# Performance work log

Measured on AMD Instinct MI355X. Metric: run time of the kernel, lower is better.

## Reference

```python
import jax, jax.numpy as jnp
import numpy as np

H = 1024; NH = 16; L = 4; K = 128; N = 65536
ADIM_MOVE = 9; ADIM_TURN = 4; S = 2 * K + 2


def setup_inputs() -> dict:
    key = jax.random.key(0)
    ks = jax.random.split(key, 24)
    s = 0.02
    d = {}
    d['x'] = jax.random.normal(ks[0], (1, H), jnp.float32)
    d['memory_vectors'] = jax.random.normal(ks[1], (N, H), jnp.float32)
    d['memory_next_vectors'] = jax.random.normal(ks[2], (N, H), jnp.float32)
    d['memory_surprises'] = jax.random.uniform(ks[3], (N,), jnp.float32)
    d['memory_rewards'] = jax.random.normal(ks[4], (N,), jnp.float32)
    d['rand_noise'] = jax.random.uniform(ks[5], (N,), jnp.float32)
    d['action_idx_move'] = jax.random.randint(ks[6], (N,), 0, ADIM_MOVE)
    d['action_idx_turn'] = jax.random.randint(ks[7], (N,), 0, ADIM_TURN)
    d['start_token'] = jax.random.uniform(ks[8], (1, H)) * 2 - 1
    d['pos_emb'] = jax.random.uniform(ks[9], (S, H)) * 2 - 1
    d['in_proj_w'] = jax.random.normal(ks[10], (L, 3 * H, H)) * s
    d['in_proj_b'] = jnp.zeros((L, 3 * H))
    d['out_w'] = jax.random.normal(ks[11], (L, H, H)) * s
    d['out_b'] = jnp.zeros((L, H))
    d['ln1_w'] = jnp.ones((L, H)); d['ln1_b'] = jnp.zeros((L, H))
    d['ln2_w'] = jnp.ones((L, H)); d['ln2_b'] = jnp.zeros((L, H))
    d['ffn_w1'] = jax.random.normal(ks[12], (L, 4 * H, H)) * s
    d['ffn_b1'] = jnp.zeros((L, 4 * H))
    d['ffn_w2'] = jax.random.normal(ks[13], (L, H, 4 * H)) * s
    d['ffn_b2'] = jnp.zeros((L, H))
    d['act_move_w1'] = jax.random.normal(ks[14], (H, ADIM_MOVE)) * s
    d['act_move_b1'] = jnp.zeros((H,))
    d['act_move_w2'] = jax.random.normal(ks[15], (H, H)) * s
    d['act_move_b2'] = jnp.zeros((H,))
    d['act_turn_w1'] = jax.random.normal(ks[16], (H, ADIM_TURN)) * s
    d['act_turn_b1'] = jnp.zeros((H,))
    d['act_turn_w2'] = jax.random.normal(ks[17], (H, H)) * s
    d['act_turn_b2'] = jnp.zeros((H,))
    d['vh_w1'] = jax.random.normal(ks[18], (4 * H, H)) * s
    d['vh_b1'] = jnp.zeros((4 * H,))
    d['vh_w2'] = jax.random.normal(ks[19], (1, 4 * H)) * s
    d['vh_b2'] = jnp.zeros((1,))
    return d


def _get_scores(v):
    # tie-aware average rank / N (matches torch unique_consecutive logic)
    srt = jnp.sort(v)
    left = jnp.searchsorted(srt, v, side='left')
    right = jnp.searchsorted(srt, v, side='right')
    return ((left + right - 1).astype(v.dtype) / 2) / v.shape[0]


def _ln(x, w, b):
    m = x.mean(-1, keepdims=True)
    var = ((x - m) ** 2).mean(-1, keepdims=True)
    return (x - m) / jnp.sqrt(var + 1e-5) * w + b


def _gelu(x):
    return jax.nn.gelu(x, approximate=False)


def _mha(x, wqkv, bqkv, wo, bo, mask):
    dh = H // NH
    qkv = x @ wqkv.T + bqkv                      # [S, 3H]
    q, k, v = jnp.split(qkv, 3, axis=-1)
    q = q.reshape(-1, NH, dh); k = k.reshape(-1, NH, dh); v = v.reshape(-1, NH, dh)
    att = jnp.einsum('qhd,khd->hqk', q, k) / np.sqrt(dh).astype(np.float32)
    att = jax.nn.softmax(att + mask, axis=-1)
    o = jnp.einsum('hqk,khd->qhd', att, v).reshape(-1, H)
    return o @ wo.T + bo


def reference(x, memory_vectors, memory_next_vectors, memory_surprises, memory_rewards, rand_noise, action_idx_move, action_idx_turn, start_token, pos_emb, in_proj_w, in_proj_b, out_w, out_b, ln1_w, ln1_b, ln2_w, ln2_b, ffn_w1, ffn_b1, ffn_w2, ffn_b2, act_move_w1, act_move_b1, act_move_w2, act_move_b2, act_turn_w1, act_turn_b1, act_turn_w2, act_turn_b2, vh_w1, vh_b1, vh_w2, vh_b2):
    eps = 1e-8
    # ---- scoring (no_grad in original) ----
    xs = jax.lax.stop_gradient(x)
    xn = xs / jnp.maximum(jnp.linalg.norm(xs, axis=-1, keepdims=True), eps)
    mn = memory_vectors / jnp.maximum(jnp.linalg.norm(memory_vectors, axis=-1, keepdims=True), eps)
    sim = mn @ xn[0]                              # [N]
    scores = _get_scores(memory_surprises) ** 2 + _get_scores(sim) ** 2 + _get_scores(rand_noise) ** 2
    _, idx = jax.lax.top_k(scores, K)             # [K]
    # ---- gather memories + action one-hots ----
    sel = jax.lax.stop_gradient(memory_vectors[idx])   # [K, H]
    oh_move = jax.nn.one_hot(action_idx_move[idx], ADIM_MOVE, dtype=x.dtype)
    oh_turn = jax.nn.one_hot(action_idx_turn[idx], ADIM_TURN, dtype=x.dtype)
    av_move = _gelu(oh_move @ act_move_w1.T + act_move_b1) @ act_move_w2.T + act_move_b2
    av_turn = _gelu(oh_turn @ act_turn_w1.T + act_turn_b1) @ act_turn_w2.T + act_turn_b2
    av = (av_move + av_turn) / 2                  # mean over actions
    # interleave [v0, a0, v1, a1, ...], prepend start, append target
    vecs = jnp.stack((sel, av), axis=1).reshape(-1, H)
    vecs = jnp.concatenate((start_token, vecs, x), axis=0)   # [S, H]
    vecs = vecs + pos_emb
    mask = jnp.where(jnp.tril(jnp.ones((S, S), bool)), 0.0, -jnp.inf).astype(x.dtype)
    for l in range(L):
        vecs = vecs + _mha(_ln(vecs, ln1_w[l], ln1_b[l]), in_proj_w[l], in_proj_b[l], out_w[l], out_b[l], mask)
        h = _ln(vecs, ln2_w[l], ln2_b[l])
        vecs = vecs + _gelu(h @ ffn_w1[l].T + ffn_b1[l]) @ ffn_w2[l].T + ffn_b2[l]
    vidx = jnp.arange(K + 1) * 2 + 1
    vh_in = vecs[vidx]
    vp = _gelu(vh_in @ vh_w1.T + vh_b1) @ vh_w2.T + vh_b2   # [K+1, 1]
    sel_rewards = memory_rewards[idx]
    losses = (vp[:-1].ravel() - sel_rewards) ** 2            # mse, reduction='none'
    return (vecs[1:], memory_next_vectors[idx], vp[-1], losses, sel_rewards)
```

## Files before the change

### kernel.cpp

```cpp
#include <hip/hip_runtime.h>
#include <hip/hip_bf16.h>
#include <math.h>
#include <stdint.h>

typedef unsigned int u32;
typedef unsigned short u16;
typedef unsigned long long u64;

#define NM   65536
#define HD   1024
#define KS   128
#define SQ   258
#define NL   4
#define NBIN 65536
#define CCAP 2048

using bf16x8 = __attribute__((ext_vector_type(8))) short;
using f32x4v = __attribute__((ext_vector_type(4))) float;

static constexpr size_t A256(size_t x){ return (x + 255) & ~(size_t)255; }

constexpr size_t OFF_H3   = 0;
constexpr size_t OFF_C3   = OFF_H3 + (size_t)3*NBIN*4;
constexpr size_t OFF_HS   = OFF_C3 + (size_t)3*NBIN*4;
constexpr size_t ZERO_BYTES = OFF_HS + (size_t)NBIN*4;
constexpr u32 ZBLK = 1792;
constexpr size_t OFF_BS   = A256(ZERO_BYTES);
constexpr size_t OFF_P3   = A256(OFF_BS + 192*4);
constexpr size_t OFF_K3   = A256(OFF_P3 + (size_t)3*(NBIN+1)*4);
constexpr size_t OFF_L3   = A256(OFF_K3 + (size_t)3*NM*4);
constexpr size_t OFF_KSC  = A256(OFF_L3 + (size_t)3*NM*4);
constexpr size_t OFF_IDX  = A256(OFF_KSC + (size_t)NM*4);
constexpr size_t OFF_REW  = A256(OFF_IDX  + (size_t)KS*4);
constexpr size_t OFF_HM   = A256(OFF_REW  + (size_t)KS*4);
constexpr size_t OFF_HT   = A256(OFF_HM   + (size_t)KS*HD*2);
constexpr size_t OFF_VECS = A256(OFF_HT   + (size_t)KS*HD*2);
constexpr size_t OFF_LNB  = A256(OFF_VECS + (size_t)SQ*HD*4);
constexpr size_t OFF_QKV  = A256(OFF_LNB  + (size_t)SQ*HD*2);
constexpr size_t OFF_ATT  = A256(OFF_QKV  + (size_t)SQ*3*HD*2);
constexpr size_t OFF_FFH  = A256(OFF_ATT  + (size_t)SQ*HD*2);
constexpr size_t OFF_VHIN = A256(OFF_FFH  + (size_t)SQ*4*HD*2);
constexpr size_t OFF_WB   = A256(OFF_VHIN + (size_t)129*HD*2);
constexpr size_t NWELEM   = 56623104;
constexpr size_t OFF_PART = A256(OFF_WB + NWELEM*2);

constexpr size_t WB_IN = 0;
constexpr size_t WB_O  = WB_IN + (size_t)4*3*HD*HD;
constexpr size_t WB_F1 = WB_O  + (size_t)4*HD*HD;
constexpr size_t WB_F2 = WB_F1 + (size_t)4*4*HD*HD;
constexpr size_t WB_AM = WB_F2 + (size_t)4*4*HD*HD;
constexpr size_t WB_AT = WB_AM + (size_t)HD*HD;
constexpr size_t WB_VH = WB_AT + (size_t)HD*HD;

constexpr int OUT_NEXT = 257*HD;
constexpr int OUT_VP   = OUT_NEXT + KS*HD;
constexpr int OUT_LOSS = OUT_VP + 1;
constexpr int OUT_REWO = OUT_LOSS + KS;

struct Ctrl { u32 b1, above1, T, candcnt; };

__device__ __forceinline__ float gelu_f(float v){
  return 0.5f*v*(1.0f + erff(v*0.70710678118654752440f));
}

__device__ __forceinline__ u16 f2bf(float f){
  __hip_bfloat16 h = __float2bfloat16(f);
  u16 s; __builtin_memcpy(&s, &h, sizeof(u16));
  return s;
}

__device__ __forceinline__ float bf2f(u16 v){ return __uint_as_float(((u32)v) << 16); }

__device__ __forceinline__ float4 unpk4(u64 pk){
  u32 lo = (u32)pk, hi = (u32)(pk >> 32);
  float4 v;
  v.x = __uint_as_float(lo << 16);
  v.y = __uint_as_float(lo & 0xFFFF0000u);
  v.z = __uint_as_float(hi << 16);
  v.w = __uint_as_float(hi & 0xFFFF0000u);
  return v;
}

__device__ __forceinline__ u64 pk4(float4 v){
  u16 r[4] = { f2bf(v.x), f2bf(v.y), f2bf(v.z), f2bf(v.w) };
  u64 pk; __builtin_memcpy(&pk, r, 8);
  return pk;
}

__device__ __forceinline__ u32 fkey(float v){
  u32 b = __float_as_uint(v);
  return (b >> 31) ? ~b : (b | 0x80000000u);
}

__device__ __forceinline__ void gload16(const u16* g, u16* l){
  __builtin_amdgcn_global_load_lds(
      (const __attribute__((address_space(1))) unsigned int*)g,
      (__attribute__((address_space(3))) unsigned int*)l, 16, 0, 0);
}

struct WSeg { const float* s; u16* d; u32 base4, end4; };
struct WCA { WSeg seg[7]; u32 tot4; u32* z; };
__global__ __launch_bounds__(256) void k_wconv(WCA a){
  if(blockIdx.x < ZBLK) a.z[blockIdx.x*256 + threadIdx.x] = 0u;
  u32 i = blockIdx.x*256 + threadIdx.x;
  if(i >= a.tot4) return;
  #pragma unroll
  for(int j=0;j<7;++j){
    if(i < a.seg[j].end4){
      u32 off = i - a.seg[j].base4;
      float4 v = *(const float4*)&a.seg[j].s[(size_t)off*4];
      *(u64*)&a.seg[j].d[(size_t)off*4] = pk4(v);
      return;
    }
  }
}

__global__ __launch_bounds__(256) void k_simkey(const float* __restrict__ mv, const float* __restrict__ x,
                                                const float* __restrict__ surp, const float* __restrict__ noise,
                                                u32* __restrict__ keys3, u32* __restrict__ hist3){
  __shared__ float xs[HD];
  __shared__ float red[256];
  int t = threadIdx.x;
  float s = 0.f;
  for(int i=t;i<HD;i+=256){ float v=x[i]; s += v*v; }
  red[t]=s; __syncthreads();
  for(int o=128;o>0;o>>=1){ if(t<o) red[t]+=red[t+o]; __syncthreads(); }
  float nrm = fmaxf(sqrtf(red[0]), 1e-8f);
  for(int i=t;i<HD;i+=256) xs[i] = x[i]/nrm;
  __syncthreads();
  int lane = t & 63, w = t >> 6;
  #pragma unroll
  for(int rep=0;rep<2;++rep){
    int row = blockIdx.x*8 + rep*4 + w;
    const float4* p = (const float4*)(mv + (size_t)row*HD);
    const float4* q = (const float4*)xs;
    float d=0.f, ss=0.f;
    #pragma unroll
    for(int r=0;r<4;++r){
      float4 v = p[lane + 64*r]; float4 u = q[lane + 64*r];
      d  += v.x*u.x + v.y*u.y + v.z*u.z + v.w*u.w;
      ss += v.x*v.x + v.y*v.y + v.z*v.z + v.w*v.w;
    }
    for(int off=32;off>0;off>>=1){ d += __shfl_xor(d,off,64); ss += __shfl_xor(ss,off,64); }
    if(lane==0){
      float sim = d / fmaxf(sqrtf(ss),1e-8f);
      float vals[3] = { surp[row], sim, noise[row] };
      #pragma unroll
      for(int a=0;a<3;++a){
        u32 k = fkey(vals[a]);
        keys3[(size_t)a*NM + row] = k;
        atomicAdd(&hist3[(size_t)a*NBIN + (k >> 16)], 1u);
      }
    }
  }
}

__global__ __launch_bounds__(256) void k_scanA(const u32* __restrict__ hist3, u32* __restrict__ bsum){
  __shared__ u32 red[256];
  int blk = blockIdx.x;
  int t = threadIdx.x;
  const u32* h = hist3 + (size_t)(blk>>6)*NBIN + (size_t)(blk&63)*1024;
  u32 s = 0;
  #pragma unroll
  for(int j=0;j<4;++j) s += h[t*4+j];
  red[t]=s; __syncthreads();
  for(int o=128;o>0;o>>=1){ if(t<o) red[t]+=red[t+o]; __syncthreads(); }
  if(t==0) bsum[blk] = red[0];
}

__global__ __launch_bounds__(256) void k_scanC(const u32* __restrict__ hist3, const u32* __restrict__ bsum,
                                               u32* __restrict__ pref3){
  __shared__ u32 part[256];
  int blk = blockIdx.x;
  int t = threadIdx.x;
  int a = blk >> 6, c = blk & 63;
  u32 base = 0;
  for(int j=0;j<c;++j) base += bsum[a*64 + j];
  const u32* h = hist3 + (size_t)a*NBIN + (size_t)c*1024;
  u32* pref = pref3 + (size_t)a*(NBIN+1) + (size_t)c*1024;
  u32 loc[4]; u32 s = 0;
  #pragma unroll
  for(int j=0;j<4;++j){ loc[j] = h[t*4+j]; s += loc[j]; }
  part[t] = s; __syncthreads();
  for(int off=1;off<256;off<<=1){
    u32 u = (t >= off) ? part[t-off] : 0u;
    __syncthreads(); part[t] += u; __syncthreads();
  }
  u32 run = base + part[t] - s;
  #pragma unroll
  for(int j=0;j<4;++j){ pref[t*4+j] = run; run += loc[j]; }
  if(c == 63 && t == 255) pref3[(size_t)a*(NBIN+1) + NBIN] = NM;
}

__global__ void k_scatter3(const u32* __restrict__ keys3, const u32* __restrict__ pref3,
                           u32* __restrict__ cnt3, u32* __restrict__ lo3){
  int i = blockIdx.x*256 + threadIdx.x;
  if(i >= NM) return;
  #pragma unroll
  for(int a=0;a<3;++a){
    u32 k = keys3[(size_t)a*NM + i];
    u32 b = k >> 16;
    u32 pos = pref3[(size_t)a*(NBIN+1) + b] + atomicAdd(&cnt3[(size_t)a*NBIN + b], 1u);
    lo3[(size_t)a*NM + pos] = k & 0xFFFFu;
  }
}

__global__ void k_rank3score(const u32* __restrict__ keys3, const u32* __restrict__ pref3,
                             const u32* __restrict__ lo3, u32* __restrict__ keysS, u32* __restrict__ histS){
  int i = blockIdx.x*256 + threadIdx.x;
  if(i >= NM) return;
  float rr[3];
  #pragma unroll
  for(int a=0;a<3;++a){
    u32 k = keys3[(size_t)a*NM + i];
    u32 b = k >> 16, my = k & 0xFFFFu;
    const u32* pref = pref3 + (size_t)a*(NBIN+1);
    const u32* lo = lo3 + (size_t)a*NM;
    u32 s = pref[b], e = pref[b+1];
    u32 nl = 0, ne = 0;
    for(u32 j=s;j<e;++j){ u32 u = lo[j]; nl += (u < my); ne += (u == my); }
    u32 left = s + nl, right = left + ne;
    rr[a] = (float)(left + right - 1) * (1.0f/131072.0f);
  }
  float sc = __fadd_rn(__fadd_rn(__fmul_rn(rr[0],rr[0]), __fmul_rn(rr[1],rr[1])), __fmul_rn(rr[2],rr[2]));
  u32 k = __float_as_uint(sc);
  keysS[i] = k;
  atomicAdd(&histS[k >> 16], 1u);
}

__global__ __launch_bounds__(1024) void k_selsort(const u32* __restrict__ histS, const u32* __restrict__ keysS,
                                                  int* __restrict__ idx){
  __shared__ u32 part[1024];
  __shared__ u64 sm[CCAP];
  __shared__ u32 thrT, cnt;
  int t = threadIdx.x;
  u32 base = t*64, s = 0;
  for(int j=0;j<64;++j) s += histS[base+j];
  part[t] = s; __syncthreads();
  for(int off=1;off<1024;off<<=1){
    u32 v = (t+off < 1024) ? part[t+off] : 0u;
    __syncthreads(); part[t] += v; __syncthreads();
  }
  u32 above = part[t] - s;
  if(above < (u32)KS && above + s >= (u32)KS){
    u32 cum = above;
    for(int j=63;j>=0;--j){
      u32 c = histS[base+j];
      if(cum + c >= (u32)KS){ thrT = (u32)(base+j) << 16; cnt = 0; break; }
      cum += c;
    }
  }
  __syncthreads();
  u32 T = thrT;
  for(int i=t;i<NM;i+=1024){
    u32 k = keysS[i];
    if(k >= T){
      u32 p = atomicAdd(&cnt, 1u);
      if(p < (u32)CCAP) sm[p] = ((u64)(~k) << 32) | (u32)i;
    }
  }
  __syncthreads();
  u32 n = cnt; if(n > (u32)CCAP) n = CCAP;
  for(int i=t;i<CCAP;i+=1024) if(i >= (int)n) sm[i] = 0xFFFFFFFFFFFFFFFFull;
  __syncthreads();
  for(int k=2;k<=CCAP;k<<=1){
    for(int j=k>>1;j>0;j>>=1){
      for(int i=t;i<CCAP;i+=1024){
        int ixj = i ^ j;
        if(ixj > i){
          bool up = ((i & k) == 0);
          u64 a = sm[i], b = sm[ixj];
          if((a > b) == up){ sm[i] = b; sm[ixj] = a; }
        }
      }
      __syncthreads();
    }
  }
  if(t < KS) idx[t] = (int)(sm[t] & 0xFFFFFFFFu);
}

__global__ void k_gather(const int* __restrict__ idx,
                         const float* __restrict__ mv, const float* __restrict__ mnv,
                         const float* __restrict__ mrew,
                         const int* __restrict__ aim, const int* __restrict__ ait,
                         const float* __restrict__ amw1, const float* __restrict__ amb1,
                         const float* __restrict__ atw1, const float* __restrict__ atb1,
                         const float* __restrict__ start, const float* __restrict__ x,
                         const float* __restrict__ pos,
                         float* __restrict__ vecs, float* __restrict__ outnext,
                         u16* __restrict__ hm, u16* __restrict__ ht,
                         float* __restrict__ rew, float* __restrict__ outrew){
  int k = blockIdx.x;
  int t = threadIdx.x;
  if(k < KS){
    int row = idx[k];
    const float4* a = (const float4*)(mv  + (size_t)row*HD);
    const float4* b = (const float4*)(mnv + (size_t)row*HD);
    const float4* pz = (const float4*)(pos + (size_t)(2*k+1)*HD);
    float4* vr = (float4*)(vecs + (size_t)(2*k+1)*HD);
    float4* on = (float4*)(outnext + (size_t)k*HD);
    float4 av = a[t], bv = b[t], pv = pz[t];
    av.x += pv.x; av.y += pv.y; av.z += pv.z; av.w += pv.w;
    vr[t] = av; on[t] = bv;
    int am = aim[row], at = ait[row];
    for(int j=t;j<HD;j+=256){
      hm[(size_t)k*HD+j] = f2bf(gelu_f(amw1[(size_t)j*9 + am] + amb1[j]));
      ht[(size_t)k*HD+j] = f2bf(gelu_f(atw1[(size_t)j*4 + at] + atb1[j]));
    }
    if(t == 0){ float r = mrew[row]; rew[k] = r; outrew[k] = r; }
  } else {
    const float4* st = (const float4*)start;
    const float4* xx = (const float4*)x;
    const float4* p0 = (const float4*)pos;
    const float4* p1 = (const float4*)(pos + (size_t)(SQ-1)*HD);
    float4 v0 = st[t], v1 = xx[t], q0 = p0[t], q1 = p1[t];
    v0.x += q0.x; v0.y += q0.y; v0.z += q0.z; v0.w += q0.w;
    v1.x += q1.x; v1.y += q1.y; v1.z += q1.z; v1.w += q1.w;
    ((float4*)vecs)[t] = v0;
    ((float4*)(vecs + (size_t)(SQ-1)*HD))[t] = v1;
  }
}

__device__ __forceinline__ void gemm_body(u16* As, u16* Bs, const u16* __restrict__ A, const u16* __restrict__ B,
        u16* __restrict__ P, int M, int N, int K, int S, int nbm, int lda, int tile){
  int bm = (tile % nbm) * 64;
  int tmp = tile / nbm;
  int z  = tmp % S;
  int bn = (tmp / S) * 64;
  int Ks = K / S, kbeg = z*Ks;
  int nk = Ks >> 5;

  int t = threadIdx.x, lane = t & 63, w = t >> 6;
  int srow = w*16 + (lane >> 2);
  int clog = (lane & 3) ^ ((srow >> 1) & 3);
  const u16* ga = A + (size_t)(bm + srow)*lda + kbeg + clog*8;
  const u16* gb = B + (size_t)(bn + srow)*K  + kbeg + clog*8;
  u16* la = As + w*512;
  u16* lb = Bs + w*512;

  int wm = (w >> 1)*32, wn = (w & 1)*32;
  int lr = lane & 15, lg = lane >> 4;
  int r0 = wm + lr, r1 = r0 + 16;
  int c0 = wn + lr, c1 = c0 + 16;
  int aoff0 = r0*32 + ((lg ^ ((r0>>1)&3))*8);
  int aoff1 = r1*32 + ((lg ^ ((r1>>1)&3))*8);
  int boff0 = c0*32 + ((lg ^ ((c0>>1)&3))*8);
  int boff1 = c1*32 + ((lg ^ ((c1>>1)&3))*8);

  f32x4v acc00 = {0,0,0,0}, acc01 = {0,0,0,0}, acc10 = {0,0,0,0}, acc11 = {0,0,0,0};

  gload16(ga, la);
  gload16(gb, lb);
  ga += 32; gb += 32;
  __syncthreads();

  for(int kk = 0; kk < nk; ++kk){
    int cur = (kk & 1) * 2048;
    if(kk + 1 < nk){
      int nxt = 2048 - cur;
      gload16(ga, la + nxt);
      gload16(gb, lb + nxt);
      ga += 32; gb += 32;
    }
    bf16x8 a0 = *(const bf16x8*)&As[cur + aoff0];
    bf16x8 a1 = *(const bf16x8*)&As[cur + aoff1];
    bf16x8 b0 = *(const bf16x8*)&Bs[cur + boff0];
    bf16x8 b1 = *(const bf16x8*)&Bs[cur + boff1];
    acc00 = __builtin_amdgcn_mfma_f32_16x16x32_bf16(a0, b0, acc00, 0, 0, 0);
    acc01 = __builtin_amdgcn_mfma_f32_16x16x32_bf16(a0, b1, acc01, 0, 0, 0);
    acc10 = __builtin_amdgcn_mfma_f32_16x16x32_bf16(a1, b0, acc10, 0, 0, 0);
    acc11 = __builtin_amdgcn_mfma_f32_16x16x32_bf16(a1, b1, acc11, 0, 0, 0);
    __syncthreads();
  }

  size_t zbase = (size_t)z * (size_t)M;
  #pragma unroll
  for(int r=0;r<4;++r){
    int row0 = bm + wm + lg*4 + r;
    int row1 = row0 + 16;
    int cc0 = bn + wn + lr, cc1 = cc0 + 16;
    if(row0 < M){
      P[(zbase+row0)*N + cc0] = f2bf(acc00[r]);
      P[(zbase+row0)*N + cc1] = f2bf(acc01[r]);
    }
    if(row1 < M){
      P[(zbase+row1)*N + cc0] = f2bf(acc10[r]);
      P[(zbase+row1)*N + cc1] = f2bf(acc11[r]);
    }
  }
}

__global__ __launch_bounds__(256) void k_gemm(const u16* __restrict__ A, const u16* __restrict__ B,
        u16* __restrict__ P, int M, int N, int K, int S, int nbm, int lda){
  __shared__ u16 As[4096];
  __shared__ u16 Bs[4096];
  u32 nwg = gridDim.x, orig = blockIdx.x;
  u32 swz = (orig & 7)*(nwg >> 3) + (orig >> 3);
  gemm_body(As, Bs, A, B, P, M, N, K, S, nbm, lda, (int)swz);
}

__global__ __launch_bounds__(256) void k_actgemm(const u16* __restrict__ hm, const u16* __restrict__ ht,
        const u16* __restrict__ amw2, const u16* __restrict__ atw2,
        u16* __restrict__ part, u16* __restrict__ part2){
  __shared__ u16 As[4096];
  __shared__ u16 Bs[4096];
  int which = blockIdx.x >> 8, tile = blockIdx.x & 255;
  gemm_body(As, Bs, which ? ht : hm, which ? atw2 : amw2, which ? part2 : part,
            KS, HD, HD, 8, 2, HD, tile);
}

template<int S_, int ACT, bool BFOUT>
__global__ __launch_bounds__(256) void k_finS(const u16* __restrict__ P, const float* __restrict__ bias,
                                              float* __restrict__ C, u16* __restrict__ Cb, int MN4, int Nd){
  int i4 = blockIdx.x*256 + threadIdx.x;
  if(i4 >= MN4) return;
  size_t off = (size_t)i4*4;
  size_t MN = (size_t)MN4*4;
  float4 v = unpk4(*(const u64*)&P[off]);
  #pragma unroll
  for(int z=1;z<S_;++z){
    float4 q = unpk4(*(const u64*)&P[(size_t)z*MN + off]);
    v.x += q.x; v.y += q.y; v.z += q.z; v.w += q.w;
  }
  int j = (i4 % (Nd/4))*4;
  float4 b4 = *(const float4*)&bias[j];
  v.x += b4.x; v.y += b4.y; v.z += b4.z; v.w += b4.w;
  if(ACT == 1){ v.x = gelu_f(v.x); v.y = gelu_f(v.y); v.z = gelu_f(v.z); v.w = gelu_f(v.w); }
  if(BFOUT) *(u64*)&Cb[off] = pk4(v);
  else      *(float4*)&C[off] = v;
}

template<int S_, bool LN>
__global__ __launch_bounds__(256) void k_finrow(const u16* __restrict__ P, const float* __restrict__ bias,
                                                float* __restrict__ vecs, const float* __restrict__ lw,
                                                const float* __restrict__ lb, u16* __restrict__ lnb,
                                                float* __restrict__ outp, u16* __restrict__ vhin){
  __shared__ float red[256];
  int row = blockIdx.x, t = threadIdx.x;
  int j = t*4;
  float4 v = unpk4(*(const u64*)&P[(size_t)row*HD + j]);
  #pragma unroll
  for(int z=1;z<S_;++z){
    float4 p = unpk4(*(const u64*)&P[((size_t)z*SQ + row)*HD + j]);
    v.x += p.x; v.y += p.y; v.z += p.z; v.w += p.w;
  }
  float4 b4 = *(const float4*)&bias[j];
  float4 r4 = *(const float4*)&vecs[(size_t)row*HD + j];
  v.x += b4.x + r4.x; v.y += b4.y + r4.y; v.z += b4.z + r4.z; v.w += b4.w + r4.w;
  *(float4*)&vecs[(size_t)row*HD + j] = v;
  if(LN){
    red[t] = v.x+v.y+v.z+v.w; __syncthreads();
    for(int o=128;o>0;o>>=1){ if(t<o) red[t]+=red[t+o]; __syncthreads(); }
    float m = red[0]*(1.0f/HD); __syncthreads();
    float dx=v.x-m, dy=v.y-m, dz=v.z-m, dw=v.w-m;
    red[t] = dx*dx+dy*dy+dz*dz+dw*dw; __syncthreads();
    for(int o=128;o>0;o>>=1){ if(t<o) red[t]+=red[t+o]; __syncthreads(); }
    float den = sqrtf(red[0]*(1.0f/HD) + 1e-5f);
    float4 w4 = *(const float4*)&lw[j];
    float4 lb4 = *(const float4*)&lb[j];
    float4 o4;
    o4.x = dx/den*w4.x + lb4.x; o4.y = dy/den*w4.y + lb4.y;
    o4.z = dz/den*w4.z + lb4.z; o4.w = dw/den*w4.w + lb4.w;
    *(u64*)&lnb[(size_t)row*HD + j] = pk4(o4);
  } else {
    if(row >= 1) *(float4*)&outp[(size_t)(row-1)*HD + j] = v;
    if(row & 1){
      int vr = (row-1) >> 1;
      *(u64*)&vhin[(size_t)vr*HD + j] = pk4(v);
    }
  }
}

__global__ __launch_bounds__(256) void k_finavln(const u16* __restrict__ Pm, const u16* __restrict__ Pt,
                                                 const float* __restrict__ bm_, const float* __restrict__ bt_,
                                                 const float* __restrict__ pos, float* __restrict__ vecs,
                                                 const float* __restrict__ lw, const float* __restrict__ lb,
                                                 u16* __restrict__ lnb){
  __shared__ float red[256];
  int row = blockIdx.x, t = threadIdx.x;
  int j = t*4;
  float4 v;
  if(row >= 2 && row <= 256 && ((row & 1) == 0)){
    int k = (row-2) >> 1;
    float4 s = {0,0,0,0};
    #pragma unroll
    for(int z=0;z<8;++z){
      float4 a = unpk4(*(const u64*)&Pm[((size_t)z*KS + k)*HD + j]);
      float4 b = unpk4(*(const u64*)&Pt[((size_t)z*KS + k)*HD + j]);
      s.x += a.x+b.x; s.y += a.y+b.y; s.z += a.z+b.z; s.w += a.w+b.w;
    }
    float4 bm4 = *(const float4*)&bm_[j];
    float4 bt4 = *(const float4*)&bt_[j];
    float4 p4 = *(const float4*)&pos[(size_t)row*HD + j];
    v.x = 0.5f*(s.x + bm4.x + bt4.x) + p4.x;
    v.y = 0.5f*(s.y + bm4.y + bt4.y) + p4.y;
    v.z = 0.5f*(s.z + bm4.z + bt4.z) + p4.z;
    v.w = 0.5f*(s.w + bm4.w + bt4.w) + p4.w;
    *(float4*)&vecs[(size_t)row*HD + j] = v;
  } else {
    v = *(const float4*)&vecs[(size_t)row*HD + j];
  }
  red[t] = v.x+v.y+v.z+v.w; __syncthreads();
  for(int o=128;o>0;o>>=1){ if(t<o) red[t]+=red[t+o]; __syncthreads(); }
  float m = red[0]*(1.0f/HD); __syncthreads();
  float dx=v.x-m, dy=v.y-m, dz=v.z-m, dw=v.w-m;
  red[t] = dx*dx+dy*dy+dz*dz+dw*dw; __syncthreads();
  for(int o=128;o>0;o>>=1){ if(t<o) red[t]+=red[t+o]; __syncthreads(); }
  float den = sqrtf(red[0]*(1.0f/HD) + 1e-5f);
  float4 w4 = *(const float4*)&lw[j];
  float4 lb4 = *(const float4*)&lb[j];
  float4 o4;
  o4.x = dx/den*w4.x + lb4.x; o4.y = dy/den*w4.y + lb4.y;
  o4.z = dz/den*w4.z + lb4.z; o4.w = dw/den*w4.w + lb4.w;
  *(u64*)&lnb[(size_t)row*HD + j] = pk4(o4);
}

__global__ void k_attn(const u16* __restrict__ qkv, u16* __restrict__ outp){
  __shared__ float qv[64];
  __shared__ float p[SQ];
  __shared__ float red[256];
  int q = blockIdx.x, h = blockIdx.y, t = threadIdx.x;
  if(t < 64) qv[t] = bf2f(qkv[(size_t)q*3072 + h*64 + t]);
  __syncthreads();
  int nk = q + 1;
  float lmax = -1e30f;
  for(int j=t;j<nk;j+=256){
    const u32* kr = (const u32*)(qkv + (size_t)j*3072 + 1024 + h*64);
    float d = 0.f;
    #pragma unroll
    for(int c2=0;c2<32;++c2){
      u32 pk = kr[c2];
      d += qv[c2*2]   * __uint_as_float(pk << 16);
      d += qv[c2*2+1] * __uint_as_float(pk & 0xFFFF0000u);
    }
    d *= 0.125f;
    p[j] = d;
    lmax = fmaxf(lmax, d);
  }
  red[t] = lmax; __syncthreads();
  for(int o=128;o>0;o>>=1){ if(t<o) red[t] = fmaxf(red[t], red[t+o]); __syncthreads(); }
  float m = red[0];
  __syncthreads();
  float lsum = 0.f;
  for(int j=t;j<nk;j+=256){ float e = expf(p[j]-m); p[j] = e; lsum += e; }
  red[t] = lsum; __syncthreads();
  for(int o=128;o>0;o>>=1){ if(t<o) red[t] += red[t+o]; __syncthreads(); }
  float inv = 1.0f/red[0];
  __syncthreads();
  int d = t & 63, g = t >> 6;
  float acc = 0.f;
  for(int j=g;j<nk;j+=4) acc += p[j]*bf2f(qkv[(size_t)j*3072 + 2048 + h*64 + d]);
  red[t] = acc; __syncthreads();
  if(g == 0){
    float o4 = red[d] + red[64+d] + red[128+d] + red[192+d];
    outp[(size_t)q*HD + h*64 + d] = f2bf(o4*inv);
  }
}

__global__ __launch_bounds__(256) void k_vpfin(const u16* __restrict__ P, const float* __restrict__ vb1,
                                               const float* __restrict__ vw2, const float* __restrict__ vb2,
                                               const float* __restrict__ rew, float* __restrict__ outp){
  __shared__ float red[256];
  int r = blockIdx.x, t = threadIdx.x;
  float s = 0.f;
  for(int c4=t;c4<1024;c4+=256){
    float4 v = unpk4(*(const u64*)&P[(size_t)r*4096 + c4*4]);
    #pragma unroll
    for(int z=1;z<4;++z){
      float4 q = unpk4(*(const u64*)&P[((size_t)z*129 + r)*4096 + c4*4]);
      v.x += q.x; v.y += q.y; v.z += q.z; v.w += q.w;
    }
    float4 b4 = *(const float4*)&vb1[c4*4];
    float4 w4 = *(const float4*)&vw2[c4*4];
    s += gelu_f(v.x + b4.x)*w4.x + gelu_f(v.y + b4.y)*w4.y
       + gelu_f(v.z + b4.z)*w4.z + gelu_f(v.w + b4.w)*w4.w;
  }
  red[t]=s; __syncthreads();
  for(int o=128;o>0;o>>=1){ if(t<o) red[t]+=red[t+o]; __syncthreads(); }
  if(t == 0){
    float val = red[0] + vb2[0];
    if(r == KS) outp[OUT_VP] = val;
    else { float d = val - rew[r]; outp[OUT_LOSS + r] = d*d; }
  }
}

extern "C" void kernel_launch(void* const* d_in, const int* in_sizes, int n_in,
                              void* d_out, int out_size, void* d_ws, size_t ws_size,
                              hipStream_t stream){
  const float* x     = (const float*)d_in[0];
  const float* mv    = (const float*)d_in[1];
  const float* mnv   = (const float*)d_in[2];
  const float* surp  = (const float*)d_in[3];
  const float* mrew  = (const float*)d_in[4];
  const float* noise = (const float*)d_in[5];
  const int*   aim   = (const int*)d_in[6];
  const int*   ait   = (const int*)d_in[7];
  const float* start = (const float*)d_in[8];
  const float* pos   = (const float*)d_in[9];
  const float* inW = (const float*)d_in[10]; const float* inB = (const float*)d_in[11];
  const float* oW  = (const float*)d_in[12]; const float* oB  = (const float*)d_in[13];
  const float* l1w = (const float*)d_in[14]; const float* l1b = (const float*)d_in[15];
  const float* l2w = (const float*)d_in[16]; const float* l2b = (const float*)d_in[17];
  const float* f1w = (const float*)d_in[18]; const float* f1b = (const float*)d_in[19];
  const float* f2w = (const float*)d_in[20]; const float* f2b = (const float*)d_in[21];
  const float* amw1= (const float*)d_in[22]; const float* amb1= (const float*)d_in[23];
  const float* amw2= (const float*)d_in[24]; const float* amb2= (const float*)d_in[25];
  const float* atw1= (const float*)d_in[26]; const float* atb1= (const float*)d_in[27];
  const float* atw2= (const float*)d_in[28]; const float* atb2= (const float*)d_in[29];
  const float* vw1 = (const float*)d_in[30]; const float* vb1 = (const float*)d_in[31];
  const float* vw2 = (const float*)d_in[32]; const float* vb2 = (const float*)d_in[33];

  float* out = (float*)d_out;
  char* ws = (char*)d_ws;
  u32*  hist3 = (u32*)(ws+OFF_H3);
  u32*  cnt3  = (u32*)(ws+OFF_C3);
  u32*  histS = (u32*)(ws+OFF_HS);
  u32*  bsum  = (u32*)(ws+OFF_BS);
  u32*  pref3 = (u32*)(ws+OFF_P3);
  u32*  keys3 = (u32*)(ws+OFF_K3);
  u32*  lo3   = (u32*)(ws+OFF_L3);
  u32*  keysS = (u32*)(ws+OFF_KSC);
  int*  idxb  = (int*)(ws+OFF_IDX);
  float* rew  = (float*)(ws+OFF_REW);
  u16*  hm    = (u16*)(ws+OFF_HM);
  u16*  ht    = (u16*)(ws+OFF_HT);
  float* vecs = (float*)(ws+OFF_VECS);
  u16*  lnb   = (u16*)(ws+OFF_LNB);
  u16*  qkvb  = (u16*)(ws+OFF_QKV);
  u16*  attn  = (u16*)(ws+OFF_ATT);
  u16*  ffh   = (u16*)(ws+OFF_FFH);
  u16*  vhin  = (u16*)(ws+OFF_VHIN);
  u16*  wb    = (u16*)(ws+OFF_WB);
  u16*  part  = (u16*)(ws+OFF_PART);
  u16*  part2 = part + (size_t)8*KS*HD;

  u16* inW_bf = wb + WB_IN;
  u16* oW_bf  = wb + WB_O;
  u16* f1w_bf = wb + WB_F1;
  u16* f2w_bf = wb + WB_F2;
  u16* am_bf  = wb + WB_AM;
  u16* at_bf  = wb + WB_AT;
  u16* vh_bf  = wb + WB_VH;

  dim3 b256(256);
  int gN = NM/256;

  {
    WCA a;
    const float* srcs[7] = { inW, oW, f1w, f2w, amw2, atw2, vw1 };
    u16* dsts[7] = { inW_bf, oW_bf, f1w_bf, f2w_bf, am_bf, at_bf, vh_bf };
    u32 sizes4[7] = { 4*3*HD*HD/4, 4*HD*HD/4, 4*4*HD*HD/4, 4*4*HD*HD/4, HD*HD/4, HD*HD/4, 4*HD*HD/4 };
    u32 cum = 0;
    for(int j=0;j<7;++j){
      a.seg[j].s = srcs[j]; a.seg[j].d = dsts[j];
      a.seg[j].base4 = cum; cum += sizes4[j]; a.seg[j].end4 = cum;
    }
    a.tot4 = cum;
    a.z = (u32*)ws;
    hipLaunchKernelGGL(k_wconv, dim3((cum + 255)/256), b256, 0, stream, a);
  }

  hipLaunchKernelGGL(k_simkey, dim3(NM/8), b256, 0, stream, mv, x, surp, noise, keys3, hist3);
  hipLaunchKernelGGL(k_scanA, dim3(192), b256, 0, stream, hist3, bsum);
  hipLaunchKernelGGL(k_scanC, dim3(192), b256, 0, stream, hist3, bsum, pref3);
  hipLaunchKernelGGL(k_scatter3, dim3(gN), b256, 0, stream, keys3, pref3, cnt3, lo3);
  hipLaunchKernelGGL(k_rank3score, dim3(gN), b256, 0, stream, keys3, pref3, lo3, keysS, histS);
  hipLaunchKernelGGL(k_selsort, dim3(1), dim3(1024), 0, stream, histS, keysS, idxb);

  hipLaunchKernelGGL(k_gather, dim3(KS+1), b256, 0, stream, idxb, mv, mnv, mrew, aim, ait,
                     amw1, amb1, atw1, atb1, start, x, pos,
                     vecs, out + OUT_NEXT, hm, ht, rew, out + OUT_REWO);
  hipLaunchKernelGGL(k_actgemm, dim3(512), b256, 0, stream, hm, ht, am_bf, at_bf, part, part2);
  hipLaunchKernelGGL(k_finavln, dim3(SQ), b256, 0, stream, part, part2, amb2, atb2, pos, vecs, l1w, l1b, lnb);

  for(int l=0;l<NL;++l){
    hipLaunchKernelGGL(k_gemm, dim3(480), b256, 0, stream, lnb, inW_bf + (size_t)l*3*HD*HD, part, SQ, 3*HD, HD, 2, 5, HD);
    hipLaunchKernelGGL((k_finS<2,0,true>), dim3(774), b256, 0, stream, part, inB + (size_t)l*3*HD, (float*)nullptr, qkvb, SQ*3*HD/4, 3*HD);
    hipLaunchKernelGGL(k_attn, dim3(SQ, 16), b256, 0, stream, qkvb, attn);
    hipLaunchKernelGGL(k_gemm, dim3(640), b256, 0, stream, attn, oW_bf + (size_t)l*HD*HD, part, SQ, HD, HD, 8, 5, HD);
    hipLaunchKernelGGL((k_finrow<8,true>), dim3(SQ), b256, 0, stream, part, oB + (size_t)l*HD, vecs,
                       l2w + (size_t)l*HD, l2b + (size_t)l*HD, lnb, (float*)nullptr, (u16*)nullptr);
    hipLaunchKernelGGL(k_gemm, dim3(640), b256, 0, stream, lnb, f1w_bf + (size_t)l*4*HD*HD, part, SQ, 4*HD, HD, 2, 5, HD);
    hipLaunchKernelGGL((k_finS<2,1,true>), dim3(1032), b256, 0, stream, part, f1b + (size_t)l*4*HD, (float*)nullptr, ffh, SQ*4*HD/4, 4*HD);
    hipLaunchKernelGGL(k_gemm, dim3(640), b256, 0, stream, ffh, f2w_bf + (size_t)l*HD*4*HD, part, SQ, HD, 4*HD, 8, 5, 4*HD);
    if(l < NL-1)
      hipLaunchKernelGGL((k_finrow<8,true>), dim3(SQ), b256, 0, stream, part, f2b + (size_t)l*HD, vecs,
                         l1w + (size_t)(l+1)*HD, l1b + (size_t)(l+1)*HD, lnb, (float*)nullptr, (u16*)nullptr);
    else
      hipLaunchKernelGGL((k_finrow<8,false>), dim3(SQ), b256, 0, stream, part, f2b + (size_t)l*HD, vecs,
                         (const float*)nullptr, (const float*)nullptr, (u16*)nullptr, out, vhin);
  }

  hipLaunchKernelGGL(k_gemm, dim3(768), b256, 0, stream, vhin, vh_bf, part, KS+1, 4*HD, HD, 4, 3, HD);
  hipLaunchKernelGGL(k_vpfin, dim3(KS+1), b256, 0, stream, part, vb1, vw2, vb2, rew, out);
}
```

Before: 883.0 us.

## Double GEMM K-step to 64 and store sorted low key halves as u16

The shared GEMM body now stages 64-wide K slices per iteration: two 16-byte loads per thread per operand, an 8-way XOR swizzle, and two MFMA rounds between barriers. This halves the number of barrier/prefetch iterations and doubles LDS per block. Separately, the low 16 bits of the rank-sort keys are stored as u16 instead of u32, halving scatter and scan traffic in the rank kernel. The larger LDS footprint may reduce occupancy, and split-K depths must now be multiples of 64.

```diff
diff --git a/kernel.cpp b/kernel.cpp
--- a/kernel.cpp
+++ b/kernel.cpp
@@ -29,7 +29,7 @@
 constexpr size_t OFF_P3   = A256(OFF_BS + 192*4);
 constexpr size_t OFF_K3   = A256(OFF_P3 + (size_t)3*(NBIN+1)*4);
 constexpr size_t OFF_L3   = A256(OFF_K3 + (size_t)3*NM*4);
-constexpr size_t OFF_KSC  = A256(OFF_L3 + (size_t)3*NM*4);
+constexpr size_t OFF_KSC  = A256(OFF_L3 + (size_t)3*NM*2);
 constexpr size_t OFF_IDX  = A256(OFF_KSC + (size_t)NM*4);
 constexpr size_t OFF_REW  = A256(OFF_IDX  + (size_t)KS*4);
 constexpr size_t OFF_HM   = A256(OFF_REW  + (size_t)KS*4);
@@ -56,8 +56,6 @@
 constexpr int OUT_VP   = OUT_NEXT + KS*HD;
 constexpr int OUT_LOSS = OUT_VP + 1;
 constexpr int OUT_REWO = OUT_LOSS + KS;
-
-struct Ctrl { u32 b1, above1, T, candcnt; };
 
 __device__ __forceinline__ float gelu_f(float v){
   return 0.5f*v*(1.0f + erff(v*0.70710678118654752440f));
@@ -193,7 +191,7 @@
 }
 
 __global__ void k_scatter3(const u32* __restrict__ keys3, const u32* __restrict__ pref3,
-                           u32* __restrict__ cnt3, u32* __restrict__ lo3){
+                           u32* __restrict__ cnt3, u16* __restrict__ lo3){
   int i = blockIdx.x*256 + threadIdx.x;
   if(i >= NM) return;
   #pragma unroll
@@ -201,12 +199,12 @@
     u32 k = keys3[(size_t)a*NM + i];
     u32 b = k >> 16;
     u32 pos = pref3[(size_t)a*(NBIN+1) + b] + atomicAdd(&cnt3[(size_t)a*NBIN + b], 1u);
-    lo3[(size_t)a*NM + pos] = k & 0xFFFFu;
+    lo3[(size_t)a*NM + pos] = (u16)(k & 0xFFFFu);
   }
 }
 
 __global__ void k_rank3score(const u32* __restrict__ keys3, const u32* __restrict__ pref3,
-                             const u32* __restrict__ lo3, u32* __restrict__ keysS, u32* __restrict__ histS){
+                             const u16* __restrict__ lo3, u32* __restrict__ keysS, u32* __restrict__ histS){
   int i = blockIdx.x*256 + threadIdx.x;
   if(i >= NM) return;
   float rr[3];
@@ -215,7 +213,7 @@
     u32 k = keys3[(size_t)a*NM + i];
     u32 b = k >> 16, my = k & 0xFFFFu;
     const u32* pref = pref3 + (size_t)a*(NBIN+1);
-    const u32* lo = lo3 + (size_t)a*NM;
+    const u16* lo = lo3 + (size_t)a*NM;
     u32 s = pref[b], e = pref[b+1];
     u32 nl = 0, ne = 0;
     for(u32 j=s;j<e;++j){ u32 u = lo[j]; nl += (u < my); ne += (u == my); }
@@ -328,48 +326,62 @@
   int z  = tmp % S;
   int bn = (tmp / S) * 64;
   int Ks = K / S, kbeg = z*Ks;
-  int nk = Ks >> 5;
+  int nk = Ks >> 6;
 
   int t = threadIdx.x, lane = t & 63, w = t >> 6;
-  int srow = w*16 + (lane >> 2);
-  int clog = (lane & 3) ^ ((srow >> 1) & 3);
-  const u16* ga = A + (size_t)(bm + srow)*lda + kbeg + clog*8;
-  const u16* gb = B + (size_t)(bn + srow)*K  + kbeg + clog*8;
-  u16* la = As + w*512;
-  u16* lb = Bs + w*512;
+  int s0 = w*64 + lane, s1 = s0 + 256;
+  int r0s = s0 >> 3, c0s = (s0 & 7) ^ (r0s & 7);
+  int r1s = s1 >> 3, c1s = (s1 & 7) ^ (r1s & 7);
+  const u16* ga0 = A + (size_t)(bm + r0s)*lda + kbeg + c0s*8;
+  const u16* ga1 = A + (size_t)(bm + r1s)*lda + kbeg + c1s*8;
+  const u16* gb0 = B + (size_t)(bn + r0s)*K  + kbeg + c0s*8;
+  const u16* gb1 = B + (size_t)(bn + r1s)*K  + kbeg + c1s*8;
+  int lb0 = w*512, lb1 = 2048 + w*512;
 
   int wm = (w >> 1)*32, wn = (w & 1)*32;
   int lr = lane & 15, lg = lane >> 4;
-  int r0 = wm + lr, r1 = r0 + 16;
-  int c0 = wn + lr, c1 = c0 + 16;
-  int aoff0 = r0*32 + ((lg ^ ((r0>>1)&3))*8);
-  int aoff1 = r1*32 + ((lg ^ ((r1>>1)&3))*8);
-  int boff0 = c0*32 + ((lg ^ ((c0>>1)&3))*8);
-  int boff1 = c1*32 + ((lg ^ ((c1>>1)&3))*8);
+  int ra0 = wm + lr, ra1 = ra0 + 16;
+  int rb0 = wn + lr, rb1 = rb0 + 16;
+  int a00 = ra0*64 + ((lg     ^ (ra0&7))*8);
+  int a01 = ra0*64 + (((4+lg) ^ (ra0&7))*8);
+  int a10 = ra1*64 + ((lg     ^ (ra1&7))*8);
+  int a11 = ra1*64 + (((4+lg) ^ (ra1&7))*8);
+  int b00 = rb0*64 + ((lg     ^ (rb0&7))*8);
+  int b01 = rb0*64 + (((4+lg) ^ (rb0&7))*8);
+  int b10 = rb1*64 + ((lg     ^ (rb1&7))*8);
+  int b11 = rb1*64 + (((4+lg) ^ (rb1&7))*8);
 
   f32x4v acc00 = {0,0,0,0}, acc01 = {0,0,0,0}, acc10 = {0,0,0,0}, acc11 = {0,0,0,0};
 
-  gload16(ga, la);
-  gload16(gb, lb);
-  ga += 32; gb += 32;
+  gload16(ga0, As + lb0); gload16(ga1, As + lb1);
+  gload16(gb0, Bs + lb0); gload16(gb1, Bs + lb1);
+  ga0 += 64; ga1 += 64; gb0 += 64; gb1 += 64;
   __syncthreads();
 
   for(int kk = 0; kk < nk; ++kk){
-    int cur = (kk & 1) * 2048;
+    int cur = (kk & 1) << 12;
     if(kk + 1 < nk){
-      int nxt = 2048 - cur;
-      gload16(ga, la + nxt);
-      gload16(gb, lb + nxt);
-      ga += 32; gb += 32;
-    }
-    bf16x8 a0 = *(const bf16x8*)&As[cur + aoff0];
-    bf16x8 a1 = *(const bf16x8*)&As[cur + aoff1];
-    bf16x8 b0 = *(const bf16x8*)&Bs[cur + boff0];
-    bf16x8 b1 = *(const bf16x8*)&Bs[cur + boff1];
-    acc00 = __builtin_amdgcn_mfma_f32_16x16x32_bf16(a0, b0, acc00, 0, 0, 0);
-    acc01 = __builtin_amdgcn_mfma_f32_16x16x32_bf16(a0, b1, acc01, 0, 0, 0);
-    acc10 = __builtin_amdgcn_mfma_f32_16x16x32_bf16(a1, b0, acc10, 0, 0, 0);
-    acc11 = __builtin_amdgcn_mfma_f32_16x16x32_bf16(a1, b1, acc11, 0, 0, 0);
+      int nxt = cur ^ 4096;
+      gload16(ga0, As + nxt + lb0); gload16(ga1, As + nxt + lb1);
+      gload16(gb0, Bs + nxt + lb0); gload16(gb1, Bs + nxt + lb1);
+      ga0 += 64; ga1 += 64; gb0 += 64; gb1 += 64;
+    }
+    bf16x8 xa0 = *(const bf16x8*)&As[cur + a00];
+    bf16x8 xa1 = *(const bf16x8*)&As[cur + a10];
+    bf16x8 xb0 = *(const bf16x8*)&Bs[cur + b00];
+    bf16x8 xb1 = *(const bf16x8*)&Bs[cur + b10];
+    acc00 = __builtin_amdgcn_mfma_f32_16x16x32_bf16(xa0, xb0, acc00, 0, 0, 0);
+    acc01 = __builtin_amdgcn_mfma_f32_16x16x32_bf16(xa0, xb1, acc01, 0, 0, 0);
+    acc10 = __builtin_amdgcn_mfma_f32_16x16x32_bf16(xa1, xb0, acc10, 0, 0, 0);
+    acc11 = __builtin_amdgcn_mfma_f32_16x16x32_bf16(xa1, xb1, acc11, 0, 0, 0);
+    xa0 = *(const bf16x8*)&As[cur + a01];
+    xa1 = *(const bf16x8*)&As[cur + a11];
+    xb0 = *(const bf16x8*)&Bs[cur + b01];
+    xb1 = *(const bf16x8*)&Bs[cur + b11];
+    acc00 = __builtin_amdgcn_mfma_f32_16x16x32_bf16(xa0, xb0, acc00, 0, 0, 0);
+    acc01 = __builtin_amdgcn_mfma_f32_16x16x32_bf16(xa0, xb1, acc01, 0, 0, 0);
+    acc10 = __builtin_amdgcn_mfma_f32_16x16x32_bf16(xa1, xb0, acc10, 0, 0, 0);
+    acc11 = __builtin_amdgcn_mfma_f32_16x16x32_bf16(xa1, xb1, acc11, 0, 0, 0);
     __syncthreads();
   }
 
@@ -392,8 +404,8 @@
 
 __global__ __launch_bounds__(256) void k_gemm(const u16* __restrict__ A, const u16* __restrict__ B,
         u16* __restrict__ P, int M, int N, int K, int S, int nbm, int lda){
-  __shared__ u16 As[4096];
-  __shared__ u16 Bs[4096];
+  __shared__ u16 As[8192];
+  __shared__ u16 Bs[8192];
   u32 nwg = gridDim.x, orig = blockIdx.x;
   u32 swz = (orig & 7)*(nwg >> 3) + (orig >> 3);
   gemm_body(As, Bs, A, B, P, M, N, K, S, nbm, lda, (int)swz);
@@ -402,8 +414,8 @@
 __global__ __launch_bounds__(256) void k_actgemm(const u16* __restrict__ hm, const u16* __restrict__ ht,
         const u16* __restrict__ amw2, const u16* __restrict__ atw2,
         u16* __restrict__ part, u16* __restrict__ part2){
-  __shared__ u16 As[4096];
-  __shared__ u16 Bs[4096];
+  __shared__ u16 As[8192];
+  __shared__ u16 Bs[8192];
   int which = blockIdx.x >> 8, tile = blockIdx.x & 255;
   gemm_body(As, Bs, which ? ht : hm, which ? atw2 : amw2, which ? part2 : part,
             KS, HD, HD, 8, 2, HD, tile);
@@ -618,7 +630,7 @@
   u32*  bsum  = (u32*)(ws+OFF_BS);
   u32*  pref3 = (u32*)(ws+OFF_P3);
   u32*  keys3 = (u32*)(ws+OFF_K3);
-  u32*  lo3   = (u32*)(ws+OFF_L3);
+  u16*  lo3   = (u16*)(ws+OFF_L3);
   u32*  keysS = (u32*)(ws+OFF_KSC);
   int*  idxb  = (int*)(ws+OFF_IDX);
   float* rew  = (float*)(ws+OFF_REW);
```

Result: faster. 850.5 us (-3.7%).
